# Kernel tuning notes

Measured on AMD Instinct MI355X. Metric: run time of the kernel, lower is better.

The kernel has to match this reference:

```python
import jax, jax.numpy as jnp
import numpy as np

N_NODES = 100000
N_EDGES = 800000
NODE_SIZE = 128
HIDDEN = 64
HEADS = 3
NEG_SLOPE = 0.2  # DGL GATConv default negative_slope


def setup_inputs() -> dict:
    key = jax.random.key(0)
    ks = jax.random.split(key, 12)
    h = jax.random.normal(ks[0], (N_NODES, NODE_SIZE), dtype=jnp.float32)
    src = jax.random.randint(ks[1], (N_EDGES,), 0, N_NODES, dtype=jnp.int32)
    dst = jax.random.randint(ks[2], (N_EDGES,), 0, N_NODES, dtype=jnp.int32)
    def glorot(k, shape):
        fan = shape[0] + shape[-1]
        return jax.random.normal(k, shape, dtype=jnp.float32) * jnp.sqrt(2.0 / fan)
    # layer 0: node_size -> hidden, 3 heads
    W0 = glorot(ks[3], (NODE_SIZE, HEADS * HIDDEN))
    al0 = glorot(ks[4], (HEADS, HIDDEN))
    ar0 = glorot(ks[5], (HEADS, HIDDEN))
    b0 = jnp.zeros((HEADS * HIDDEN,), dtype=jnp.float32)
    # layer 1: hidden -> hidden, 3 heads
    W1 = glorot(ks[6], (HIDDEN, HEADS * HIDDEN))
    al1 = glorot(ks[7], (HEADS, HIDDEN))
    ar1 = glorot(ks[8], (HEADS, HIDDEN))
    b1 = jnp.zeros((HEADS * HIDDEN,), dtype=jnp.float32)
    return {"h": h, "src": src, "dst": dst,
            "W0": W0, "al0": al0, "ar0": ar0, "b0": b0,
            "W1": W1, "al1": al1, "ar1": ar1, "b1": b1}


def _gat_layer(x, src, dst, W, al, ar, b):
    """DGL GATConv (allow_zero_in_degree=True, bias=True) followed by head mean."""
    n = x.shape[0]
    z = (x @ W).reshape(n, HEADS, HIDDEN)                 # [N,H,F]
    el = jnp.einsum('nhf,hf->nh', z, al)                  # [N,H]
    er = jnp.einsum('nhf,hf->nh', z, ar)                  # [N,H]
    e = jax.nn.leaky_relu(el[src] + er[dst], NEG_SLOPE)   # [E,H]
    # segment-wise (per-dst) stable softmax over variable-degree neighborhoods
    m = jax.ops.segment_max(e, dst, num_segments=n)       # [N,H]
    a = jnp.exp(e - m[dst])                               # [E,H]
    s = jax.ops.segment_sum(a, dst, num_segments=n)       # [N,H]
    alpha = a / s[dst]                                    # [E,H]
    msg = alpha[:, :, None] * z[src]                      # [E,H,F]
    out = jax.ops.segment_sum(msg, dst, num_segments=n)   # [N,H,F]
    out = out + b.reshape(1, HEADS, HIDDEN)
    return out.mean(axis=1)                               # head mean -> [N,F]


def reference(h, src, dst, W0, al0, ar0, b0, W1, al1, ar1, b1):
    h1 = _gat_layer(h, src, dst, W0, al0, ar0, b0)
    h1 = _gat_layer(h1, src, dst, W1, al1, ar1, b1)
    # dgl.mean_nodes: graph readout (single graph -> mean over all nodes)
    return h1.mean(axis=0)                                # [HIDDEN]
```

## Files before the change

### kernel.cpp

```cpp
#include <hip/hip_runtime.h>
#include <hip/hip_bf16.h>

#define HEADS 3
#define HID 64
#define OUTW (HEADS * HID)
#define NS 128
#define NB_LSUM 2048

typedef __attribute__((ext_vector_type(8))) short bf16x8;
typedef __attribute__((ext_vector_type(4))) float f32x4;

__device__ __forceinline__ float lrelu(float x) {
    return x > 0.f ? x : 0.2f * x;
}

__device__ __forceinline__ unsigned short f2bf(float f) {
    unsigned u = __float_as_uint(f);
    u += 0x7fff + ((u >> 16) & 1);
    return (unsigned short)(u >> 16);
}

__device__ __forceinline__ float bf2f(unsigned short u) {
    return __uint_as_float((unsigned)u << 16);
}


__global__ void k_zero_int(int* p, int n) {
    int i = blockIdx.x * blockDim.x + threadIdx.x;
    for (; i < n; i += gridDim.x * blockDim.x) p[i] = 0;
}

__global__ void k_hist(const int* __restrict__ key, int* __restrict__ cnt, int E) {
    int i = blockIdx.x * blockDim.x + threadIdx.x;
    for (; i < E; i += gridDim.x * blockDim.x) atomicAdd(&cnt[key[i]], 1);
}

__global__ void k_scan1(const int* __restrict__ cnt, int* __restrict__ rowstart,
                        int* __restrict__ blocksums, int N) {
    int t = threadIdx.x;
    int base = blockIdx.x * 1024 + t * 4;
    int v[4];
    int ts = 0;
#pragma unroll
    for (int j = 0; j < 4; ++j) {
        v[j] = (base + j < N) ? cnt[base + j] : 0;
        ts += v[j];
    }
    __shared__ int sh[256];
    sh[t] = ts;
    __syncthreads();
    for (int off = 1; off < 256; off <<= 1) {
        int x = 0;
        if (t >= off) x = sh[t - off];
        __syncthreads();
        if (t >= off) sh[t] += x;
        __syncthreads();
    }
    int excl = sh[t] - ts;
    if (t == 255) blocksums[blockIdx.x] = sh[255];
    int run = excl;
#pragma unroll
    for (int j = 0; j < 4; ++j) {
        if (base + j < N) rowstart[base + j] = run;
        run += v[j];
    }
}

__global__ void k_scan2(int* blocksums, int nb) {
    if (blockIdx.x == 0 && threadIdx.x == 0) {
        int s = 0;
        for (int i = 0; i < nb; ++i) {
            int v = blocksums[i];
            blocksums[i] = s;
            s += v;
        }
    }
}

__global__ void k_scan3(int* __restrict__ rowstart, const int* __restrict__ blocksums,
                        int* __restrict__ cursor, int N, int E) {
    int i = blockIdx.x * blockDim.x + threadIdx.x;
    if (i < N) {
        int v = rowstart[i] + blocksums[i >> 10];
        rowstart[i] = v;
        cursor[i] = v;
    }
    if (i == 0) rowstart[N] = E;
}

__global__ void k_scatter(const int* __restrict__ val, const int* __restrict__ key,
                          int* __restrict__ cursor, int* __restrict__ outidx, int E) {
    int i = blockIdx.x * blockDim.x + threadIdx.x;
    for (; i < E; i += gridDim.x * blockDim.x) {
        int d = key[i];
        int p = atomicAdd(&cursor[d], 1);
        outidx[p] = val[i];
    }
}


__global__ void k_prep(const float* __restrict__ W1, const float* __restrict__ al1,
                       const float* __restrict__ ar1, float* __restrict__ wlr1) {
    int t = threadIdx.x;
    if (t >= 192) return;
    int k = t & 63, hh = t >> 6;
    float sl = 0.f, sr = 0.f;
#pragma unroll 8
    for (int f = 0; f < 64; ++f) {
        float w = W1[k * OUTW + hh * 64 + f];
        sl = fmaf(w, al1[hh * 64 + f], sl);
        sr = fmaf(w, ar1[hh * 64 + f], sr);
    }
    wlr1[k * 8 + hh] = sl;
    wlr1[k * 8 + 4 + hh] = sr;
}


#define LDK 136

__global__ __launch_bounds__(256) void k_gemm5(const float* __restrict__ X,
                                               const float* __restrict__ W,
                                               const float* __restrict__ al,
                                               const float* __restrict__ ar,
                                               unsigned short* __restrict__ Z16,
                                               float* __restrict__ elr, int M) {
    __shared__ __align__(16) unsigned short Xs[64][LDK];
    __shared__ __align__(16) unsigned short Ws[192][LDK];
    __shared__ float elp[4][64][8];
    const int tid = threadIdx.x;
    const int lane = tid & 63;
    const int w = tid >> 6;
    const int r0 = blockIdx.x * 64;

    if (tid < 192) {
        int col = tid;
#pragma unroll 8
        for (int kp = 0; kp < 64; ++kp) {
            float w0 = W[(2 * kp) * OUTW + col];
            float w1 = W[(2 * kp + 1) * OUTW + col];
            unsigned pack = (unsigned)f2bf(w0) | ((unsigned)f2bf(w1) << 16);
            *(unsigned*)&Ws[col][2 * kp] = pack;
        }
    }
#pragma unroll
    for (int i = 0; i < 8; ++i) {
        int id = i * 256 + tid;
        int row = id >> 5, f4 = id & 31;
        int gr = r0 + row;
        if (gr >= M) gr = M - 1;
        float4 v = *(const float4*)(X + (size_t)gr * NS + f4 * 4);
        ushort4 u;
        u.x = f2bf(v.x); u.y = f2bf(v.y); u.z = f2bf(v.z); u.w = f2bf(v.w);
        *(ushort4*)&Xs[row][f4 * 4] = u;
    }
    __syncthreads();

    const int mrow = lane & 15;
    const int kgrp = (lane >> 4) * 8;

    bf16x8 bf[3][4];
#pragma unroll
    for (int c = 0; c < 3; ++c)
#pragma unroll
        for (int kb = 0; kb < 4; ++kb)
            bf[c][kb] = *(const bf16x8*)&Ws[(c * 4 + w) * 16 + mrow][kb * 32 + kgrp];

    f32x4 acc[4][3];
#pragma unroll
    for (int rb = 0; rb < 4; ++rb)
#pragma unroll
        for (int c = 0; c < 3; ++c) acc[rb][c] = (f32x4){0.f, 0.f, 0.f, 0.f};

#pragma unroll
    for (int rb = 0; rb < 4; ++rb) {
        bf16x8 af[4];
#pragma unroll
        for (int kb = 0; kb < 4; ++kb)
            af[kb] = *(const bf16x8*)&Xs[rb * 16 + mrow][kb * 32 + kgrp];
#pragma unroll
        for (int c = 0; c < 3; ++c)
#pragma unroll
            for (int kb = 0; kb < 4; ++kb)
                acc[rb][c] = __builtin_amdgcn_mfma_f32_16x16x32_bf16(
                    af[kb], bf[c][kb], acc[rb][c], 0, 0, 0);
    }

    float alv[3], arv[3];
#pragma unroll
    for (int c = 0; c < 3; ++c) {
        alv[c] = al[c * 64 + w * 16 + mrow];
        arv[c] = ar[c * 64 + w * 16 + mrow];
    }
#pragma unroll
    for (int rb = 0; rb < 4; ++rb) {
#pragma unroll
        for (int reg = 0; reg < 4; ++reg) {
            int row = r0 + rb * 16 + (lane >> 4) * 4 + reg;
            bool live = row < M;
            float pl[3], pr[3];
#pragma unroll
            for (int c = 0; c < 3; ++c) {
                float v = acc[rb][c][reg];
                if (live) Z16[(size_t)row * OUTW + (c * 4 + w) * 16 + mrow] = f2bf(v);
                pl[c] = v * alv[c];
                pr[c] = v * arv[c];
            }
#pragma unroll
            for (int m = 1; m < 16; m <<= 1) {
#pragma unroll
                for (int c = 0; c < 3; ++c) {
                    pl[c] += __shfl_xor(pl[c], m, 64);
                    pr[c] += __shfl_xor(pr[c], m, 64);
                }
            }
            if (mrow == 0) {
                int lrow = rb * 16 + (lane >> 4) * 4 + reg;
#pragma unroll
                for (int c = 0; c < 3; ++c) {
                    elp[w][lrow][c] = pl[c];
                    elp[w][lrow][4 + c] = pr[c];
                }
            }
        }
    }
    __syncthreads();
    if (tid < 64) {
        int row = r0 + tid;
        if (row < M) {
#pragma unroll
            for (int c = 0; c < 3; ++c) {
                float el = elp[0][tid][c] + elp[1][tid][c] + elp[2][tid][c] + elp[3][tid][c];
                float er = elp[0][tid][4 + c] + elp[1][tid][4 + c] + elp[2][tid][4 + c] +
                           elp[3][tid][4 + c];
                elr[(size_t)row * 8 + c] = el;
                elr[(size_t)row * 8 + 4 + c] = er;
            }
        }
    }
}


__global__ __launch_bounds__(256) void k_agg0(const unsigned short* __restrict__ z16,
                                              const float* __restrict__ elr0,
                                              const int* __restrict__ rowstart,
                                              const int* __restrict__ csr_src,
                                              const float* __restrict__ bias,
                                              const float* __restrict__ wlr1,
                                              unsigned short* __restrict__ h1b,
                                              float* __restrict__ elr1, int N) {
    int node = blockIdx.x * 4 + (threadIdx.x >> 6);
    int lane = threadIdx.x & 63;
    if (node >= N) return;
    float4 wl4 = *(const float4*)(wlr1 + lane * 8);
    float4 wr4 = *(const float4*)(wlr1 + lane * 8 + 4);
    int s = rowstart[node], e = rowstart[node + 1];
    float4 erv = *(const float4*)(elr0 + (size_t)node * 8 + 4);
    float s0 = 0.f, s1 = 0.f, s2 = 0.f;
    float a0 = 0.f, a1 = 0.f, a2 = 0.f;
    int i = s;
    for (; i + 4 <= e; i += 4) {
        int sr0 = csr_src[i];
        int sr1 = csr_src[i + 1];
        int sr2 = csr_src[i + 2];
        int sr3 = csr_src[i + 3];
        float4 el0 = *(const float4*)(elr0 + (size_t)sr0 * 8);
        float4 el1 = *(const float4*)(elr0 + (size_t)sr1 * 8);
        float4 el2 = *(const float4*)(elr0 + (size_t)sr2 * 8);
        float4 el3 = *(const float4*)(elr0 + (size_t)sr3 * 8);
        const unsigned short* zr0 = z16 + (size_t)sr0 * OUTW;
        const unsigned short* zr1 = z16 + (size_t)sr1 * OUTW;
        const unsigned short* zr2 = z16 + (size_t)sr2 * OUTW;
        const unsigned short* zr3 = z16 + (size_t)sr3 * OUTW;
        unsigned short p00 = zr0[lane], p01 = zr0[HID + lane], p02 = zr0[2 * HID + lane];
        unsigned short p10 = zr1[lane], p11 = zr1[HID + lane], p12 = zr1[2 * HID + lane];
        unsigned short p20 = zr2[lane], p21 = zr2[HID + lane], p22 = zr2[2 * HID + lane];
        unsigned short p30 = zr3[lane], p31 = zr3[HID + lane], p32 = zr3[2 * HID + lane];
        float w00 = __expf(lrelu(el0.x + erv.x));
        float w01 = __expf(lrelu(el0.y + erv.y));
        float w02 = __expf(lrelu(el0.z + erv.z));
        float w10 = __expf(lrelu(el1.x + erv.x));
        float w11 = __expf(lrelu(el1.y + erv.y));
        float w12 = __expf(lrelu(el1.z + erv.z));
        float w20 = __expf(lrelu(el2.x + erv.x));
        float w21 = __expf(lrelu(el2.y + erv.y));
        float w22 = __expf(lrelu(el2.z + erv.z));
        float w30 = __expf(lrelu(el3.x + erv.x));
        float w31 = __expf(lrelu(el3.y + erv.y));
        float w32 = __expf(lrelu(el3.z + erv.z));
        s0 += (w00 + w10) + (w20 + w30);
        s1 += (w01 + w11) + (w21 + w31);
        s2 += (w02 + w12) + (w22 + w32);
        a0 = fmaf(w00, bf2f(p00), a0);
        a1 = fmaf(w01, bf2f(p01), a1);
        a2 = fmaf(w02, bf2f(p02), a2);
        a0 = fmaf(w10, bf2f(p10), a0);
        a1 = fmaf(w11, bf2f(p11), a1);
        a2 = fmaf(w12, bf2f(p12), a2);
        a0 = fmaf(w20, bf2f(p20), a0);
        a1 = fmaf(w21, bf2f(p21), a1);
        a2 = fmaf(w22, bf2f(p22), a2);
        a0 = fmaf(w30, bf2f(p30), a0);
        a1 = fmaf(w31, bf2f(p31), a1);
        a2 = fmaf(w32, bf2f(p32), a2);
    }
    for (; i < e; ++i) {
        int sr = csr_src[i];
        float4 elv = *(const float4*)(elr0 + (size_t)sr * 8);
        const unsigned short* zr = z16 + (size_t)sr * OUTW;
        float w0 = __expf(lrelu(elv.x + erv.x));
        float w1 = __expf(lrelu(elv.y + erv.y));
        float w2 = __expf(lrelu(elv.z + erv.z));
        s0 += w0; s1 += w1; s2 += w2;
        a0 = fmaf(w0, bf2f(zr[lane]), a0);
        a1 = fmaf(w1, bf2f(zr[HID + lane]), a1);
        a2 = fmaf(w2, bf2f(zr[2 * HID + lane]), a2);
    }
    float r = bias[lane] + bias[HID + lane] + bias[2 * HID + lane];
    if (s0 > 0.f) r += a0 / s0;
    if (s1 > 0.f) r += a1 / s1;
    if (s2 > 0.f) r += a2 / s2;
    r *= (1.f / 3.f);

    h1b[(size_t)node * HID + lane] = f2bf(r);
    float pl0 = r * wl4.x, pl1 = r * wl4.y, pl2 = r * wl4.z;
    float pr0 = r * wr4.x, pr1 = r * wr4.y, pr2 = r * wr4.z;
#pragma unroll
    for (int m = 1; m < 64; m <<= 1) {
        pl0 += __shfl_xor(pl0, m, 64);
        pl1 += __shfl_xor(pl1, m, 64);
        pl2 += __shfl_xor(pl2, m, 64);
        pr0 += __shfl_xor(pr0, m, 64);
        pr1 += __shfl_xor(pr1, m, 64);
        pr2 += __shfl_xor(pr2, m, 64);
    }
    if (lane == 0) {
        elr1[(size_t)node * 8 + 0] = pl0;
        elr1[(size_t)node * 8 + 1] = pl1;
        elr1[(size_t)node * 8 + 2] = pl2;
        elr1[(size_t)node * 8 + 4] = pr0;
        elr1[(size_t)node * 8 + 5] = pr1;
        elr1[(size_t)node * 8 + 6] = pr2;
    }
}


__global__ __launch_bounds__(256) void k_lsum(const unsigned short* __restrict__ h1b,
                                              const float* __restrict__ elr1,
                                              const int* __restrict__ rowstart,
                                              const int* __restrict__ csr_src,
                                              float* __restrict__ partial, int N) {
    int lane = threadIdx.x & 63;
    int w = threadIdx.x >> 6;
    int wid = (blockIdx.x * blockDim.x + threadIdx.x) >> 6;
    int nw = (gridDim.x * blockDim.x) >> 6;
    float g0 = 0.f, g1 = 0.f, g2 = 0.f;
    for (int node = wid; node < N; node += nw) {
        int s = rowstart[node], e = rowstart[node + 1];
        if (s == e) continue;
        float4 erv = *(const float4*)(elr1 + (size_t)node * 8 + 4);
        float s0 = 0.f, s1 = 0.f, s2 = 0.f;
        float a0 = 0.f, a1 = 0.f, a2 = 0.f;
        int i = s;
        for (; i + 4 <= e; i += 4) {
            int sr0 = csr_src[i];
            int sr1 = csr_src[i + 1];
            int sr2 = csr_src[i + 2];
            int sr3 = csr_src[i + 3];
            float4 el0 = *(const float4*)(elr1 + (size_t)sr0 * 8);
            float4 el1 = *(const float4*)(elr1 + (size_t)sr1 * 8);
            float4 el2 = *(const float4*)(elr1 + (size_t)sr2 * 8);
            float4 el3 = *(const float4*)(elr1 + (size_t)sr3 * 8);
            float v0 = bf2f(h1b[(size_t)sr0 * HID + lane]);
            float v1 = bf2f(h1b[(size_t)sr1 * HID + lane]);
            float v2 = bf2f(h1b[(size_t)sr2 * HID + lane]);
            float v3 = bf2f(h1b[(size_t)sr3 * HID + lane]);
            float w00 = __expf(lrelu(el0.x + erv.x));
            float w01 = __expf(lrelu(el0.y + erv.y));
            float w02 = __expf(lrelu(el0.z + erv.z));
            float w10 = __expf(lrelu(el1.x + erv.x));
            float w11 = __expf(lrelu(el1.y + erv.y));
            float w12 = __expf(lrelu(el1.z + erv.z));
            float w20 = __expf(lrelu(el2.x + erv.x));
            float w21 = __expf(lrelu(el2.y + erv.y));
            float w22 = __expf(lrelu(el2.z + erv.z));
            float w30 = __expf(lrelu(el3.x + erv.x));
            float w31 = __expf(lrelu(el3.y + erv.y));
            float w32 = __expf(lrelu(el3.z + erv.z));
            s0 += (w00 + w10) + (w20 + w30);
            s1 += (w01 + w11) + (w21 + w31);
            s2 += (w02 + w12) + (w22 + w32);
            a0 = fmaf(w00, v0, a0);
            a1 = fmaf(w01, v0, a1);
            a2 = fmaf(w02, v0, a2);
            a0 = fmaf(w10, v1, a0);
            a1 = fmaf(w11, v1, a1);
            a2 = fmaf(w12, v1, a2);
            a0 = fmaf(w20, v2, a0);
            a1 = fmaf(w21, v2, a1);
            a2 = fmaf(w22, v2, a2);
            a0 = fmaf(w30, v3, a0);
            a1 = fmaf(w31, v3, a1);
            a2 = fmaf(w32, v3, a2);
        }
        for (; i < e; ++i) {
            int sr = csr_src[i];
            float4 elv = *(const float4*)(elr1 + (size_t)sr * 8);
            float v = bf2f(h1b[(size_t)sr * HID + lane]);
            float w0 = __expf(lrelu(elv.x + erv.x));
            float w1 = __expf(lrelu(elv.y + erv.y));
            float w2 = __expf(lrelu(elv.z + erv.z));
            s0 += w0; s1 += w1; s2 += w2;
            a0 = fmaf(w0, v, a0);
            a1 = fmaf(w1, v, a1);
            a2 = fmaf(w2, v, a2);
        }
        if (s0 > 0.f) g0 += a0 / s0;
        if (s1 > 0.f) g1 += a1 / s1;
        if (s2 > 0.f) g2 += a2 / s2;
    }
    __shared__ float sh[4][3][64];
    sh[w][0][lane] = g0;
    sh[w][1][lane] = g1;
    sh[w][2][lane] = g2;
    __syncthreads();
    if (w == 0) {
        float t0 = sh[0][0][lane] + sh[1][0][lane] + sh[2][0][lane] + sh[3][0][lane];
        float t1 = sh[0][1][lane] + sh[1][1][lane] + sh[2][1][lane] + sh[3][1][lane];
        float t2 = sh[0][2][lane] + sh[1][2][lane] + sh[2][2][lane] + sh[3][2][lane];
        float* p = partial + (size_t)blockIdx.x * OUTW;
        p[0 * HID + lane] = t0;
        p[1 * HID + lane] = t1;
        p[2 * HID + lane] = t2;
    }
}


__global__ __launch_bounds__(256) void k_red(const float* __restrict__ partial,
                                             float* __restrict__ macc, int nb) {
    int f = blockIdx.x;
    int t = threadIdx.x;
    float s = 0.f;
    for (int b = t; b < nb; b += 256) s += partial[(size_t)b * OUTW + f];
    __shared__ float sh[256];
    sh[t] = s;
    __syncthreads();
    for (int off = 128; off > 0; off >>= 1) {
        if (t < off) sh[t] += sh[t + off];
        __syncthreads();
    }
    if (t == 0) macc[f] = sh[0];
}


__global__ void k_final(const float* __restrict__ macc, const float* __restrict__ W1,
                        const float* __restrict__ b1, float* __restrict__ out, int N) {
    int f = threadIdx.x;
    if (f >= HID) return;
    float s = 0.f;
#pragma unroll
    for (int hh = 0; hh < HEADS; ++hh)
        for (int k = 0; k < HID; ++k)
            s = fmaf(macc[hh * HID + k], W1[k * OUTW + hh * HID + f], s);
    float bb = b1[f] + b1[HID + f] + b1[2 * HID + f];
    out[f] = s / (3.0f * (float)N) + bb * (1.f / 3.f);
}


extern "C" void kernel_launch(void* const* d_in, const int* in_sizes, int n_in,
                              void* d_out, int out_size, void* d_ws, size_t ws_size,
                              hipStream_t stream) {
    const float* h   = (const float*)d_in[0];
    const int* src   = (const int*)d_in[1];
    const int* dst   = (const int*)d_in[2];
    const float* W0  = (const float*)d_in[3];
    const float* al0 = (const float*)d_in[4];
    const float* ar0 = (const float*)d_in[5];
    const float* b0  = (const float*)d_in[6];
    const float* W1  = (const float*)d_in[7];
    const float* al1 = (const float*)d_in[8];
    const float* ar1 = (const float*)d_in[9];
    const float* b1  = (const float*)d_in[10];
    float* out = (float*)d_out;

    const int N = in_sizes[0] / NS;
    const int E = in_sizes[1];

    char* ws = (char*)d_ws;
    size_t off = 0;
    auto alloc = [&](size_t bytes) {
        size_t r = off;
        off = (off + bytes + 255) & ~(size_t)255;
        return r;
    };
    unsigned short* z16 = (unsigned short*)(ws + alloc((size_t)N * OUTW * 2));
    unsigned short* h1b = (unsigned short*)(ws + alloc((size_t)N * HID * 2));
    float* elr0     = (float*)(ws + alloc((size_t)N * 8 * 4));
    float* elr1     = (float*)(ws + alloc((size_t)N * 8 * 4));
    float* partial  = (float*)(ws + alloc((size_t)NB_LSUM * OUTW * 4));
    float* macc     = (float*)(ws + alloc(OUTW * 4));
    int* cnt        = (int*)(ws + alloc((size_t)N * 4));
    int* rowstart   = (int*)(ws + alloc((size_t)(N + 1) * 4));
    int* cursor     = (int*)(ws + alloc((size_t)N * 4));
    int* csr_src    = (int*)(ws + alloc((size_t)E * 4));
    int* blocksums  = (int*)(ws + alloc(4096));
    float* wlr1     = (float*)(ws + alloc(64 * 8 * 4));

    const int nbScan = (N + 1023) / 1024;

    k_zero_int<<<256, 256, 0, stream>>>(cnt, N);
    k_hist<<<512, 256, 0, stream>>>(dst, cnt, E);
    k_scan1<<<nbScan, 256, 0, stream>>>(cnt, rowstart, blocksums, N);
    k_scan2<<<1, 64, 0, stream>>>(blocksums, nbScan);
    k_scan3<<<(N + 255) / 256, 256, 0, stream>>>(rowstart, blocksums, cursor, N, E);
    k_scatter<<<512, 256, 0, stream>>>(src, dst, cursor, csr_src, E);
    k_prep<<<1, 192, 0, stream>>>(W1, al1, ar1, wlr1);

    k_gemm5<<<(N + 63) / 64, 256, 0, stream>>>(h, W0, al0, ar0, z16, elr0, N);
    k_agg0<<<(N + 3) / 4, 256, 0, stream>>>(z16, elr0, rowstart, csr_src, b0, wlr1,
                                            h1b, elr1, N);

    k_lsum<<<NB_LSUM, 256, 0, stream>>>(h1b, elr1, rowstart, csr_src, partial, N);
    k_red<<<OUTW, 256, 0, stream>>>(partial, macc, NB_LSUM);
    k_final<<<1, 64, 0, stream>>>(macc, W1, b1, out, N);
}
```

Before: 339.3 us.

## Precompute per-edge attention weights in a separate edge-parallel kernel

Adds a k_w kernel that computes exp(leaky_relu(el[src]+er[dst])) once per edge, in CSR order, into a float4 array. For this the scatter step now also writes csr_dst. The aggregation kernels then read the weights contiguously instead of gathering elr per neighbour and computing exp in every lane. This removes the redundant exp work done by all 64 lanes of a wave and the scattered elr gathers. In exchange it adds two extra kernel launches and roughly 16 bytes written and read per edge per layer.

```diff
diff --git a/kernel.cpp b/kernel.cpp
--- a/kernel.cpp
+++ b/kernel.cpp
@@ -88,13 +88,15 @@
     if (i == 0) rowstart[N] = E;
 }
 
-__global__ void k_scatter(const int* __restrict__ val, const int* __restrict__ key,
-                          int* __restrict__ cursor, int* __restrict__ outidx, int E) {
+__global__ void k_scatter(const int* __restrict__ src, const int* __restrict__ dst,
+                          int* __restrict__ cursor, int* __restrict__ csr_src,
+                          int* __restrict__ csr_dst, int E) {
     int i = blockIdx.x * blockDim.x + threadIdx.x;
     for (; i < E; i += gridDim.x * blockDim.x) {
-        int d = key[i];
+        int d = dst[i];
         int p = atomicAdd(&cursor[d], 1);
-        outidx[p] = val[i];
+        csr_src[p] = src[i];
+        csr_dst[p] = d;
     }
 }
 
@@ -113,6 +115,25 @@
     }
     wlr1[k * 8 + hh] = sl;
     wlr1[k * 8 + 4 + hh] = sr;
+}
+
+
+__global__ __launch_bounds__(256) void k_w(const float* __restrict__ elr,
+                                           const int* __restrict__ csr_src,
+                                           const int* __restrict__ csr_dst,
+                                           float4* __restrict__ w4, int E) {
+    int i = blockIdx.x * blockDim.x + threadIdx.x;
+    for (; i < E; i += gridDim.x * blockDim.x) {
+        int s = csr_src[i], d = csr_dst[i];
+        float4 el = *(const float4*)(elr + (size_t)s * 8);
+        float4 er = *(const float4*)(elr + (size_t)d * 8 + 4);
+        float4 o;
+        o.x = __expf(lrelu(el.x + er.x));
+        o.y = __expf(lrelu(el.y + er.y));
+        o.z = __expf(lrelu(el.z + er.z));
+        o.w = 0.f;
+        w4[i] = o;
+    }
 }
 
 
@@ -241,7 +262,7 @@
 
 
 __global__ __launch_bounds__(256) void k_agg0(const unsigned short* __restrict__ z16,
-                                              const float* __restrict__ elr0,
+                                              const float4* __restrict__ w4,
                                               const int* __restrict__ rowstart,
                                               const int* __restrict__ csr_src,
                                               const float* __restrict__ bias,
@@ -254,19 +275,18 @@
     float4 wl4 = *(const float4*)(wlr1 + lane * 8);
     float4 wr4 = *(const float4*)(wlr1 + lane * 8 + 4);
     int s = rowstart[node], e = rowstart[node + 1];
-    float4 erv = *(const float4*)(elr0 + (size_t)node * 8 + 4);
     float s0 = 0.f, s1 = 0.f, s2 = 0.f;
     float a0 = 0.f, a1 = 0.f, a2 = 0.f;
     int i = s;
     for (; i + 4 <= e; i += 4) {
+        float4 w0 = w4[i];
+        float4 w1 = w4[i + 1];
+        float4 w2 = w4[i + 2];
+        float4 w3 = w4[i + 3];
         int sr0 = csr_src[i];
         int sr1 = csr_src[i + 1];
         int sr2 = csr_src[i + 2];
         int sr3 = csr_src[i + 3];
-        float4 el0 = *(const float4*)(elr0 + (size_t)sr0 * 8);
-        float4 el1 = *(const float4*)(elr0 + (size_t)sr1 * 8);
-        float4 el2 = *(const float4*)(elr0 + (size_t)sr2 * 8);
-        float4 el3 = *(const float4*)(elr0 + (size_t)sr3 * 8);
         const unsigned short* zr0 = z16 + (size_t)sr0 * OUTW;
         const unsigned short* zr1 = z16 + (size_t)sr1 * OUTW;
         const unsigned short* zr2 = z16 + (size_t)sr2 * OUTW;
@@ -275,45 +295,30 @@
         unsigned short p10 = zr1[lane], p11 = zr1[HID + lane], p12 = zr1[2 * HID + lane];
         unsigned short p20 = zr2[lane], p21 = zr2[HID + lane], p22 = zr2[2 * HID + lane];
         unsigned short p30 = zr3[lane], p31 = zr3[HID + lane], p32 = zr3[2 * HID + lane];
-        float w00 = __expf(lrelu(el0.x + erv.x));
-        float w01 = __expf(lrelu(el0.y + erv.y));
-        float w02 = __expf(lrelu(el0.z + erv.z));
-        float w10 = __expf(lrelu(el1.x + erv.x));
-        float w11 = __expf(lrelu(el1.y + erv.y));
-        float w12 = __expf(lrelu(el1.z + erv.z));
-        float w20 = __expf(lrelu(el2.x + erv.x));
-        float w21 = __expf(lrelu(el2.y + erv.y));
-        float w22 = __expf(lrelu(el2.z + erv.z));
-        float w30 = __expf(lrelu(el3.x + erv.x));
-        float w31 = __expf(lrelu(el3.y + erv.y));
-        float w32 = __expf(lrelu(el3.z + erv.z));
-        s0 += (w00 + w10) + (w20 + w30);
-        s1 += (w01 + w11) + (w21 + w31);
-        s2 += (w02 + w12) + (w22 + w32);
-        a0 = fmaf(w00, bf2f(p00), a0);
-        a1 = fmaf(w01, bf2f(p01), a1);
-        a2 = fmaf(w02, bf2f(p02), a2);
-        a0 = fmaf(w10, bf2f(p10), a0);
-        a1 = fmaf(w11, bf2f(p11), a1);
-        a2 = fmaf(w12, bf2f(p12), a2);
-        a0 = fmaf(w20, bf2f(p20), a0);
-        a1 = fmaf(w21, bf2f(p21), a1);
-        a2 = fmaf(w22, bf2f(p22), a2);
-        a0 = fmaf(w30, bf2f(p30), a0);
-        a1 = fmaf(w31, bf2f(p31), a1);
-        a2 = fmaf(w32, bf2f(p32), a2);
+        s0 += (w0.x + w1.x) + (w2.x + w3.x);
+        s1 += (w0.y + w1.y) + (w2.y + w3.y);
+        s2 += (w0.z + w1.z) + (w2.z + w3.z);
+        a0 = fmaf(w0.x, bf2f(p00), a0);
+        a1 = fmaf(w0.y, bf2f(p01), a1);
+        a2 = fmaf(w0.z, bf2f(p02), a2);
+        a0 = fmaf(w1.x, bf2f(p10), a0);
+        a1 = fmaf(w1.y, bf2f(p11), a1);
+        a2 = fmaf(w1.z, bf2f(p12), a2);
+        a0 = fmaf(w2.x, bf2f(p20), a0);
+        a1 = fmaf(w2.y, bf2f(p21), a1);
+        a2 = fmaf(w2.z, bf2f(p22), a2);
+        a0 = fmaf(w3.x, bf2f(p30), a0);
+        a1 = fmaf(w3.y, bf2f(p31), a1);
+        a2 = fmaf(w3.z, bf2f(p32), a2);
     }
     for (; i < e; ++i) {
+        float4 wv = w4[i];
         int sr = csr_src[i];
-        float4 elv = *(const float4*)(elr0 + (size_t)sr * 8);
         const unsigned short* zr = z16 + (size_t)sr * OUTW;
-        float w0 = __expf(lrelu(elv.x + erv.x));
-        float w1 = __expf(lrelu(elv.y + erv.y));
-        float w2 = __expf(lrelu(elv.z + erv.z));
-        s0 += w0; s1 += w1; s2 += w2;
-        a0 = fmaf(w0, bf2f(zr[lane]), a0);
-        a1 = fmaf(w1, bf2f(zr[HID + lane]), a1);
-        a2 = fmaf(w2, bf2f(zr[2 * HID + lane]), a2);
+        s0 += wv.x; s1 += wv.y; s2 += wv.z;
+        a0 = fmaf(wv.x, bf2f(zr[lane]), a0);
+        a1 = fmaf(wv.y, bf2f(zr[HID + lane]), a1);
+        a2 = fmaf(wv.z, bf2f(zr[2 * HID + lane]), a2);
     }
     float r = bias[lane] + bias[HID + lane] + bias[2 * HID + lane];
     if (s0 > 0.f) r += a0 / s0;
@@ -345,7 +350,7 @@
 
 
 __global__ __launch_bounds__(256) void k_lsum(const unsigned short* __restrict__ h1b,
-                                              const float* __restrict__ elr1,
+                                              const float4* __restrict__ w4,
                                               const int* __restrict__ rowstart,
                                               const int* __restrict__ csr_src,
                                               float* __restrict__ partial, int N) {
@@ -357,62 +362,46 @@
     for (int node = wid; node < N; node += nw) {
         int s = rowstart[node], e = rowstart[node + 1];
         if (s == e) continue;
-        float4 erv = *(const float4*)(elr1 + (size_t)node * 8 + 4);
         float s0 = 0.f, s1 = 0.f, s2 = 0.f;
         float a0 = 0.f, a1 = 0.f, a2 = 0.f;
         int i = s;
         for (; i + 4 <= e; i += 4) {
+            float4 w0 = w4[i];
+            float4 w1 = w4[i + 1];
+            float4 w2 = w4[i + 2];
+            float4 w3 = w4[i + 3];
             int sr0 = csr_src[i];
             int sr1 = csr_src[i + 1];
             int sr2 = csr_src[i + 2];
             int sr3 = csr_src[i + 3];
-            float4 el0 = *(const float4*)(elr1 + (size_t)sr0 * 8);
-            float4 el1 = *(const float4*)(elr1 + (size_t)sr1 * 8);
-            float4 el2 = *(const float4*)(elr1 + (size_t)sr2 * 8);
-            float4 el3 = *(const float4*)(elr1 + (size_t)sr3 * 8);
             float v0 = bf2f(h1b[(size_t)sr0 * HID + lane]);
             float v1 = bf2f(h1b[(size_t)sr1 * HID + lane]);
             float v2 = bf2f(h1b[(size_t)sr2 * HID + lane]);
             float v3 = bf2f(h1b[(size_t)sr3 * HID + lane]);
-            float w00 = __expf(lrelu(el0.x + erv.x));
-            float w01 = __expf(lrelu(el0.y + erv.y));
-            float w02 = __expf(lrelu(el0.z + erv.z));
-            float w10 = __expf(lrelu(el1.x + erv.x));
-            float w11 = __expf(lrelu(el1.y + erv.y));
-            float w12 = __expf(lrelu(el1.z + erv.z));
-            float w20 = __expf(lrelu(el2.x + erv.x));
-            float w21 = __expf(lrelu(el2.y + erv.y));
-            float w22 = __expf(lrelu(el2.z + erv.z));
-            float w30 = __expf(lrelu(el3.x + erv.x));
-            float w31 = __expf(lrelu(el3.y + erv.y));
-            float w32 = __expf(lrelu(el3.z + erv.z));
-            s0 += (w00 + w10) + (w20 + w30);
-            s1 += (w01 + w11) + (w21 + w31);
-            s2 += (w02 + w12) + (w22 + w32);
-            a0 = fmaf(w00, v0, a0);
-            a1 = fmaf(w01, v0, a1);
-            a2 = fmaf(w02, v0, a2);
-            a0 = fmaf(w10, v1, a0);
-            a1 = fmaf(w11, v1, a1);
-            a2 = fmaf(w12, v1, a2);
-            a0 = fmaf(w20, v2, a0);
-            a1 = fmaf(w21, v2, a1);
-            a2 = fmaf(w22, v2, a2);
-            a0 = fmaf(w30, v3, a0);
-            a1 = fmaf(w31, v3, a1);
-            a2 = fmaf(w32, v3, a2);
+            s0 += (w0.x + w1.x) + (w2.x + w3.x);
+            s1 += (w0.y + w1.y) + (w2.y + w3.y);
+            s2 += (w0.z + w1.z) + (w2.z + w3.z);
+            a0 = fmaf(w0.x, v0, a0);
+            a1 = fmaf(w0.y, v0, a1);
+            a2 = fmaf(w0.z, v0, a2);
+            a0 = fmaf(w1.x, v1, a0);
+            a1 = fmaf(w1.y, v1, a1);
+            a2 = fmaf(w1.z, v1, a2);
+            a0 = fmaf(w2.x, v2, a0);
+            a1 = fmaf(w2.y, v2, a1);
+            a2 = fmaf(w2.z, v2, a2);
+            a0 = fmaf(w3.x, v3, a0);
+            a1 = fmaf(w3.y, v3, a1);
+            a2 = fmaf(w3.z, v3, a2);
         }
         for (; i < e; ++i) {
+            float4 wv = w4[i];
             int sr = csr_src[i];
-            float4 elv = *(const float4*)(elr1 + (size_t)sr * 8);
             float v = bf2f(h1b[(size_t)sr * HID + lane]);
-            float w0 = __expf(lrelu(elv.x + erv.x));
-            float w1 = __expf(lrelu(elv.y + erv.y));
-            float w2 = __expf(lrelu(elv.z + erv.z));
-            s0 += w0; s1 += w1; s2 += w2;
-            a0 = fmaf(w0, v, a0);
-            a1 = fmaf(w1, v, a1);
-            a2 = fmaf(w2, v, a2);
+            s0 += wv.x; s1 += wv.y; s2 += wv.z;
+            a0 = fmaf(wv.x, v, a0);
+            a1 = fmaf(wv.y, v, a1);
+            a2 = fmaf(wv.z, v, a2);
         }
         if (s0 > 0.f) g0 += a0 / s0;
         if (s1 > 0.f) g1 += a1 / s1;
@@ -496,12 +485,15 @@
     unsigned short* h1b = (unsigned short*)(ws + alloc((size_t)N * HID * 2));
     float* elr0     = (float*)(ws + alloc((size_t)N * 8 * 4));
     float* elr1     = (float*)(ws + alloc((size_t)N * 8 * 4));
+    float4* w0arr   = (float4*)(ws + alloc((size_t)E * 16));
+    float4* w1arr   = (float4*)(ws + alloc((size_t)E * 16));
     float* partial  = (float*)(ws + alloc((size_t)NB_LSUM * OUTW * 4));
     float* macc     = (float*)(ws + alloc(OUTW * 4));
     int* cnt        = (int*)(ws + alloc((size_t)N * 4));
     int* rowstart   = (int*)(ws + alloc((size_t)(N + 1) * 4));
     int* cursor     = (int*)(ws + alloc((size_t)N * 4));
     int* csr_src    = (int*)(ws + alloc((size_t)E * 4));
+    int* csr_dst    = (int*)(ws + alloc((size_t)E * 4));
     int* blocksums  = (int*)(ws + alloc(4096));
     float* wlr1     = (float*)(ws + alloc(64 * 8 * 4));
 
@@ -512,14 +504,16 @@
     k_scan1<<<nbScan, 256, 0, stream>>>(cnt, rowstart, blocksums, N);
     k_scan2<<<1, 64, 0, stream>>>(blocksums, nbScan);
     k_scan3<<<(N + 255) / 256, 256, 0, stream>>>(rowstart, blocksums, cursor, N, E);
-    k_scatter<<<512, 256, 0, stream>>>(src, dst, cursor, csr_src, E);
+    k_scatter<<<512, 256, 0, stream>>>(src, dst, cursor, csr_src, csr_dst, E);
     k_prep<<<1, 192, 0, stream>>>(W1, al1, ar1, wlr1);
 
     k_gemm5<<<(N + 63) / 64, 256, 0, stream>>>(h, W0, al0, ar0, z16, elr0, N);
-    k_agg0<<<(N + 3) / 4, 256, 0, stream>>>(z16, elr0, rowstart, csr_src, b0, wlr1,
+    k_w<<<1024, 256, 0, stream>>>(elr0, csr_src, csr_dst, w0arr, E);
+    k_agg0<<<(N + 3) / 4, 256, 0, stream>>>(z16, w0arr, rowstart, csr_src, b0, wlr1,
                                             h1b, elr1, N);
 
-    k_lsum<<<NB_LSUM, 256, 0, stream>>>(h1b, elr1, rowstart, csr_src, partial, N);
+    k_w<<<1024, 256, 0, stream>>>(elr1, csr_src, csr_dst, w1arr, E);
+    k_lsum<<<NB_LSUM, 256, 0, stream>>>(h1b, w1arr, rowstart, csr_src, partial, N);
     k_red<<<OUTW, 256, 0, stream>>>(partial, macc, NB_LSUM);
     k_final<<<1, 64, 0, stream>>>(macc, W1, b1, out, N);
 }
```

Result: faster. 325.0 us (-4.2%).
